# Performance work log

Measured on AMD Instinct MI355X. Metric: run time of the kernel, lower is better.

The kernel has to match this reference:

```python
import jax, jax.numpy as jnp
import numpy as np

B, L, H, NL = 4, 384, 128, 3
F = H * NL  # num_filters = hidden_dim * num_layers = h_V feature dim


def gelu(x):
    return jax.nn.gelu(x, approximate=False)  # torch nn.GELU default is exact erf


def setup_inputs() -> dict:
    key = jax.random.key(0)
    ks = jax.random.split(key, 10)
    rn = lambda k, shape, s=0.05: jax.random.normal(k, shape, jnp.float32) * s
    h_V = jax.random.normal(ks[0], (B, L, F), jnp.float32)
    h_E = jax.random.normal(ks[1], (B, L, L, H), jnp.float32)
    mask = (jax.random.uniform(ks[2], (B, L)) > 0.1).astype(jnp.float32)
    # CFConv filter_network: Linear(H->F), GELU, Linear(F->F), GELU
    fw1 = rn(ks[3], (H, F)); fb1 = jnp.zeros((F,), jnp.float32)
    fw2 = rn(ks[4], (F, F)); fb2 = jnp.zeros((F,), jnp.float32)
    # mlp_head: Linear(F->H), GELU, Linear(H->H//2), GELU, Linear(H//2->1)
    hw1 = rn(ks[5], (F, H)); hb1 = jnp.zeros((H,), jnp.float32)
    hw2 = rn(ks[6], (H, H // 2)); hb2 = jnp.zeros((H // 2,), jnp.float32)
    hw3 = rn(ks[7], (H // 2, 1)); hb3 = jnp.zeros((1,), jnp.float32)
    return dict(h_V=h_V, h_E=h_E, mask=mask, fw1=fw1, fb1=fb1, fw2=fw2, fb2=fb2,
                hw1=hw1, hb1=hb1, hw2=hw2, hb2=hb2, hw3=hw3, hb3=hb3)


def reference(h_V, h_E, mask, fw1, fb1, fw2, fb2, hw1, hb1, hw2, hb2, hw3, hb3):
    # CFConv: per-edge filter MLP on edge features [B,L,L,H] -> [B,L,L,F]
    Wf = gelu(gelu(h_E @ fw1 + fb1) @ fw2 + fb2)
    # broadcast multiply with x.unsqueeze(1) then sum over neighbor dim (dim=2)
    x_conv = jnp.einsum('bkf,blkf->blf', h_V, Wf)  # [B,L,F]
    # mlp_head (dropout is identity in eval)
    h = gelu(x_conv @ hw1 + hb1)
    h = gelu(h @ hw2 + hb2)
    pred = (h @ hw3 + hb3)[..., 0]  # [B,L]
    valid_length = jnp.clip(jnp.sum(mask, axis=1), 1.0, None)
    return jnp.sum(pred * mask, axis=1) / jnp.sqrt(valid_length)  # [B]
```

## Files before the change

### kernel.cpp

```cpp
#include <hip/hip_runtime.h>


#define Bz 4
#define Lz 384
#define Hz 128
#define Fz 384
#define KT 64
#define NIT 6
#define TILE_B (KT * Hz * 2)

typedef short bf16x8 __attribute__((ext_vector_type(8)));
typedef float f32x4 __attribute__((ext_vector_type(4)));

__device__ __forceinline__ unsigned short f2bf(float f) {
  unsigned int u = __float_as_uint(f);
  u += 0x7FFFu + ((u >> 16) & 1u);
  return (unsigned short)(u >> 16);
}

__device__ __forceinline__ float gelu_f(float x) {
  const float a1 = 0.254829592f, a2 = -0.284496736f, a3 = 1.421413741f;
  const float a4 = -1.453152027f, a5 = 1.061405429f;
  float z = fabsf(x) * 0.7071067811865476f;
  float t = __builtin_amdgcn_rcpf(__builtin_fmaf(0.3275911f, z, 1.0f));
  float poly = t * (a1 + t * (a2 + t * (a3 + t * (a4 + t * a5))));
  float e = __builtin_fmaf(-poly, __expf(-z * z), 1.0f);
  return 0.5f * x * (1.0f + copysignf(e, x));
}

__global__ __launch_bounds__(256) void prep_kernel(
    const float* __restrict__ fw1, const float* __restrict__ fw2,
    const float* __restrict__ hE,
    unsigned short* __restrict__ fw1P, unsigned short* __restrict__ fw2P,
    unsigned short* __restrict__ hEP,
    float* __restrict__ accbuf, int* __restrict__ ctr)
{
  int e = blockIdx.x * 256 + threadIdx.x;
  if (e < 16) accbuf[e] = 0.0f;
  if (e == 16) *ctr = 0;
  if (e < 24 * 4 * 64 * 8) {
    int j = e & 7, lf = (e >> 3) & 63, ks = (e >> 9) & 3, t = e >> 11;
    int n = t * 16 + (lf & 15);
    int k = ks * 32 + (lf >> 4) * 8 + j;
    fw1P[e] = f2bf(fw1[(size_t)k * Fz + n]);
  } else if (e < 24 * 4 * 64 * 8 + 24 * 12 * 64 * 8) {
    int o = e - 24 * 4 * 64 * 8;
    int j = o & 7, lf = (o >> 3) & 63, r = o >> 9;
    int ks = r % 12, t = r / 12;
    int n = t * 16 + (lf & 15);
    int k = ks * 32 + (lf >> 4) * 8 + j;
    fw2P[o] = f2bf(fw2[(size_t)k * Fz + n]);
  }
  if (e < Bz * Lz * NIT * KT * 16) {
    int u = e & 15;
    int r = (e >> 4) & 63;
    int tile = e >> 10;
    int it = tile % NIT;
    int bl = tile / NIT;
    const float* src = hE + (size_t)bl * (Lz * Hz)
                       + (size_t)(it * KT + r) * Hz + ((u ^ (r & 7)) << 3);
    f32x4 v0 = *(const f32x4*)src;
    f32x4 v1 = *(const f32x4*)(src + 4);
    bf16x8 o;
    o[0] = (short)f2bf(v0[0]); o[1] = (short)f2bf(v0[1]);
    o[2] = (short)f2bf(v0[2]); o[3] = (short)f2bf(v0[3]);
    o[4] = (short)f2bf(v1[0]); o[5] = (short)f2bf(v1[1]);
    o[6] = (short)f2bf(v1[2]); o[7] = (short)f2bf(v1[3]);
    *(bf16x8*)(hEP + (size_t)e * 8) = o;
  }
}

__global__ __launch_bounds__(512, 4) void schnet_main(
    const float* __restrict__ hV, const unsigned short* __restrict__ hEP,
    const float* __restrict__ mask,
    const unsigned short* __restrict__ fw1P, const float* __restrict__ fb1,
    const unsigned short* __restrict__ fw2P, const float* __restrict__ fb2,
    const float* __restrict__ hw1, const float* __restrict__ hb1,
    const float* __restrict__ hw2, const float* __restrict__ hb2,
    const float* __restrict__ hw3, const float* __restrict__ hb3,
    float* __restrict__ accbuf, int* __restrict__ ctr,
    float* __restrict__ out)
{
  const int bl   = blockIdx.x;
  const int b    = bl / Lz;
  const int l    = bl - b * Lz;
  const int tid  = threadIdx.x;
  const int wave = tid >> 6;
  const int lane = tid & 63;
  const int lr   = lane & 15;
  const int quad = lane >> 4;
  const int l7   = lane & 7;

  __shared__ __attribute__((aligned(16))) char sMem[65536];
  unsigned short* sA  = (unsigned short*)sMem;
  unsigned short* sT1 = (unsigned short*)(sMem + 16384);
  float* sXC = (float*)sMem;
  float* sHp = sXC + Fz;
  float* sH1 = sHp + 4 * Hz;
  float* sH2 = sH1 + Hz;
  int*   sLast = (int*)(sH2 + 64);

  const char* hEPt = (const char*)hEP + (size_t)bl * (NIT * TILE_B);
  const unsigned short* w1base = fw1P + (size_t)lane * 8;
  const unsigned short* w2base = fw2P + (size_t)lane * 8;

  const f32x4 zero4 = {0.f, 0.f, 0.f, 0.f};
  f32x4 xc[3];
  xc[0] = zero4; xc[1] = zero4; xc[2] = zero4;

  #pragma unroll
  for (int j = 0; j < 2; ++j) {
    int off = (j * 8 + wave) << 10;
    __builtin_amdgcn_global_load_lds(
        (const __attribute__((address_space(1))) void*)(hEPt + off + lane * 16),
        (__attribute__((address_space(3))) void*)(sMem + off), 16, 0, 0);
  }
  __syncthreads();

  for (int it = 0; it < NIT; ++it) {
    {
      f32x4 acc[4][3];
      #pragma unroll
      for (int mt = 0; mt < 4; ++mt)
        #pragma unroll
        for (int nt = 0; nt < 3; ++nt) acc[mt][nt] = zero4;

      #pragma unroll 2
      for (int ks = 0; ks < 4; ++ks) {
        const int xu = ((ks << 2) + quad) ^ l7;
        bf16x8 afr[4];
        #pragma unroll
        for (int mt = 0; mt < 4; ++mt)
          afr[mt] = *(const bf16x8*)(sA + ((mt * 16 + lr) << 7) + (xu << 3));
        bf16x8 bfr[3];
        #pragma unroll
        for (int nt = 0; nt < 3; ++nt)
          bfr[nt] = *(const bf16x8*)(w1base +
                        (size_t)(((wave * 3 + nt) * 4 + ks) * 64) * 8);
        __builtin_amdgcn_s_setprio(1);
        #pragma unroll
        for (int mt = 0; mt < 4; ++mt)
          #pragma unroll
          for (int nt = 0; nt < 3; ++nt)
            acc[mt][nt] = __builtin_amdgcn_mfma_f32_16x16x32_bf16(
                bfr[nt], afr[mt], acc[mt][nt], 0, 0, 0);
        __builtin_amdgcn_s_setprio(0);
      }
      #pragma unroll
      for (int nt = 0; nt < 3; ++nt) {
        const int n0 = wave * 48 + nt * 16 + quad * 4;
        const f32x4 bias = *(const f32x4*)(fb1 + n0);
        const int so = (((wave * 6 + nt * 2 + (quad >> 1)) ^ l7) << 3)
                       + ((quad & 1) << 2);
        #pragma unroll
        for (int mt = 0; mt < 4; ++mt) {
          short4 o;
          o.x = (short)f2bf(gelu_f(acc[mt][nt][0] + bias[0]));
          o.y = (short)f2bf(gelu_f(acc[mt][nt][1] + bias[1]));
          o.z = (short)f2bf(gelu_f(acc[mt][nt][2] + bias[2]));
          o.w = (short)f2bf(gelu_f(acc[mt][nt][3] + bias[3]));
          *(short4*)(sT1 + (mt * 16 + lr) * 384 + so) = o;
        }
      }
    }
    __syncthreads();

    if (it + 1 < NIT) {
      const char* gt = hEPt + (it + 1) * TILE_B;
      #pragma unroll
      for (int j = 0; j < 2; ++j) {
        int off = (j * 8 + wave) << 10;
        __builtin_amdgcn_global_load_lds(
            (const __attribute__((address_space(1))) void*)(gt + off + lane * 16),
            (__attribute__((address_space(3))) void*)(sMem + off), 16, 0, 0);
      }
    }

    {
      f32x4 acc[4][3];
      #pragma unroll
      for (int mt = 0; mt < 4; ++mt)
        #pragma unroll
        for (int nt = 0; nt < 3; ++nt) acc[mt][nt] = zero4;

      #pragma unroll 2
      for (int ks = 0; ks < 12; ++ks) {
        const int xu = ((ks << 2) + quad) ^ l7;
        bf16x8 afr[4];
        #pragma unroll
        for (int mt = 0; mt < 4; ++mt)
          afr[mt] = *(const bf16x8*)(sT1 + (mt * 16 + lr) * 384 + (xu << 3));
        bf16x8 bfr[3];
        #pragma unroll
        for (int nt = 0; nt < 3; ++nt)
          bfr[nt] = *(const bf16x8*)(w2base +
                        (size_t)(((wave * 3 + nt) * 12 + ks) * 64) * 8);
        __builtin_amdgcn_s_setprio(1);
        #pragma unroll
        for (int mt = 0; mt < 4; ++mt)
          #pragma unroll
          for (int nt = 0; nt < 3; ++nt)
            acc[mt][nt] = __builtin_amdgcn_mfma_f32_16x16x32_bf16(
                bfr[nt], afr[mt], acc[mt][nt], 0, 0, 0);
        __builtin_amdgcn_s_setprio(0);
      }
      #pragma unroll
      for (int nt = 0; nt < 3; ++nt) {
        const int n0 = wave * 48 + nt * 16 + quad * 4;
        const f32x4 b2 = *(const f32x4*)(fb2 + n0);
        #pragma unroll
        for (int mt = 0; mt < 4; ++mt) {
          const float* hv =
              hV + ((size_t)b * Lz + it * KT + mt * 16 + lr) * Fz + n0;
          const f32x4 hvv = *(const f32x4*)hv;
          #pragma unroll
          for (int r = 0; r < 4; ++r)
            xc[nt][r] += gelu_f(acc[mt][nt][r] + b2[r]) * hvv[r];
        }
      }
    }
    __syncthreads();
  }

  #pragma unroll
  for (int nt = 0; nt < 3; ++nt)
    #pragma unroll
    for (int r = 0; r < 4; ++r) {
      float v = xc[nt][r];
      v += __shfl_xor(v, 1);
      v += __shfl_xor(v, 2);
      v += __shfl_xor(v, 4);
      v += __shfl_xor(v, 8);
      if (lr == 0) sXC[wave * 48 + nt * 16 + quad * 4 + r] = v;
    }
  __syncthreads();

  {
    int i = tid & 127;
    int part = tid >> 7;
    float a = 0.f;
    const int f0 = part * 96;
    for (int f = f0; f < f0 + 96; ++f) a += sXC[f] * hw1[f * Hz + i];
    sHp[part * Hz + i] = a;
  }
  __syncthreads();
  if (tid < Hz)
    sH1[tid] = gelu_f(sHp[tid] + sHp[Hz + tid] + sHp[2 * Hz + tid]
                      + sHp[3 * Hz + tid] + hb1[tid]);
  __syncthreads();
  if (tid < 64) {
    float a = hb2[tid];
    for (int i = 0; i < Hz; ++i) a += sH1[i] * hw2[i * 64 + tid];
    sH2[tid] = gelu_f(a);
  }
  __syncthreads();
  if (wave == 0) {
    float v = sH2[lane] * hw3[lane];
    #pragma unroll
    for (int off = 32; off >= 1; off >>= 1) v += __shfl_xor(v, off);
    if (lane == 0) {
      float pred = v + hb3[0];
      atomicAdd(&accbuf[b], pred * mask[b * Lz + l]);
      __threadfence();
      *sLast = (atomicAdd(ctr, 1) == (Bz * Lz - 1));
    }
  }
  __syncthreads();

  if (*sLast && wave < Bz) {
    float s = 0.f;
    #pragma unroll
    for (int k = 0; k < Lz / 64; ++k) s += mask[wave * Lz + k * 64 + lane];
    #pragma unroll
    for (int off = 32; off >= 1; off >>= 1) s += __shfl_xor(s, off);
    if (lane == 0) {
      float vl = s < 1.0f ? 1.0f : s;
      float a = atomicAdd(&accbuf[wave], 0.0f);
      out[wave] = a / sqrtf(vl);
    }
  }
}

extern "C" void kernel_launch(void* const* d_in, const int* in_sizes, int n_in,
                              void* d_out, int out_size, void* d_ws, size_t ws_size,
                              hipStream_t stream)
{
  const float* hV   = (const float*)d_in[0];
  const float* hE   = (const float*)d_in[1];
  const float* mask = (const float*)d_in[2];
  const float* fw1  = (const float*)d_in[3];
  const float* fb1  = (const float*)d_in[4];
  const float* fw2  = (const float*)d_in[5];
  const float* fb2  = (const float*)d_in[6];
  const float* hw1  = (const float*)d_in[7];
  const float* hb1  = (const float*)d_in[8];
  const float* hw2  = (const float*)d_in[9];
  const float* hb2  = (const float*)d_in[10];
  const float* hw3  = (const float*)d_in[11];
  const float* hb3  = (const float*)d_in[12];
  float* out = (float*)d_out;

  float* accbuf = (float*)d_ws;
  int*   ctr    = (int*)((char*)d_ws + 64);
  unsigned short* fw1P = (unsigned short*)((char*)d_ws + 1024);
  unsigned short* fw2P = fw1P + 24 * 4 * 64 * 8;
  unsigned short* hEP  = fw2P + 24 * 12 * 64 * 8;

  const int units = Bz * Lz * NIT * KT * 16;
  prep_kernel<<<units / 256, 256, 0, stream>>>(fw1, fw2, hE, fw1P, fw2P, hEP,
                                               accbuf, ctr);
  schnet_main<<<Bz * Lz, 512, 0, stream>>>(hV, hEP, mask, fw1P, fb1, fw2P, fb2,
                                           hw1, hb1, hw2, hb2, hw3, hb3,
                                           accbuf, ctr, out);
}
```

Measured before the change: 875.6 us.

## Fuse h_E bf16 conversion into main kernel with register-staged prefetch

Removes the separate prep pass that converted the whole h_E tensor to a swizzled bf16 buffer. The main kernel now loads fp32 h_E directly, converts it to bf16 in registers and writes it to LDS. The load for the next tile is issued before the GEMM2 phase to hide its latency. The tile size is halved to 32 rows, with 12 iterations and half the LDS, which should allow more resident blocks but doubles the number of barriers and gives less MFMA work per wave per sync.

Result: faster. 844.3 us (-3.6%).

```diff
diff --git a/kernel.cpp b/kernel.cpp
--- a/kernel.cpp
+++ b/kernel.cpp
@@ -5,9 +5,8 @@
 #define Lz 384
 #define Hz 128
 #define Fz 384
-#define KT 64
-#define NIT 6
-#define TILE_B (KT * Hz * 2)
+#define KT 32
+#define NIT 12
 
 typedef short bf16x8 __attribute__((ext_vector_type(8)));
 typedef float f32x4 __attribute__((ext_vector_type(4)));
@@ -30,9 +29,7 @@
 
 __global__ __launch_bounds__(256) void prep_kernel(
     const float* __restrict__ fw1, const float* __restrict__ fw2,
-    const float* __restrict__ hE,
     unsigned short* __restrict__ fw1P, unsigned short* __restrict__ fw2P,
-    unsigned short* __restrict__ hEP,
     float* __restrict__ accbuf, int* __restrict__ ctr)
 {
   int e = blockIdx.x * 256 + threadIdx.x;
@@ -51,27 +48,10 @@
     int k = ks * 32 + (lf >> 4) * 8 + j;
     fw2P[o] = f2bf(fw2[(size_t)k * Fz + n]);
   }
-  if (e < Bz * Lz * NIT * KT * 16) {
-    int u = e & 15;
-    int r = (e >> 4) & 63;
-    int tile = e >> 10;
-    int it = tile % NIT;
-    int bl = tile / NIT;
-    const float* src = hE + (size_t)bl * (Lz * Hz)
-                       + (size_t)(it * KT + r) * Hz + ((u ^ (r & 7)) << 3);
-    f32x4 v0 = *(const f32x4*)src;
-    f32x4 v1 = *(const f32x4*)(src + 4);
-    bf16x8 o;
-    o[0] = (short)f2bf(v0[0]); o[1] = (short)f2bf(v0[1]);
-    o[2] = (short)f2bf(v0[2]); o[3] = (short)f2bf(v0[3]);
-    o[4] = (short)f2bf(v1[0]); o[5] = (short)f2bf(v1[1]);
-    o[6] = (short)f2bf(v1[2]); o[7] = (short)f2bf(v1[3]);
-    *(bf16x8*)(hEP + (size_t)e * 8) = o;
-  }
 }
 
 __global__ __launch_bounds__(512, 4) void schnet_main(
-    const float* __restrict__ hV, const unsigned short* __restrict__ hEP,
+    const float* __restrict__ hV, const float* __restrict__ hE,
     const float* __restrict__ mask,
     const unsigned short* __restrict__ fw1P, const float* __restrict__ fb1,
     const unsigned short* __restrict__ fw2P, const float* __restrict__ fb2,
@@ -91,133 +71,146 @@
   const int quad = lane >> 4;
   const int l7   = lane & 7;
 
-  __shared__ __attribute__((aligned(16))) char sMem[65536];
+  __shared__ __attribute__((aligned(16))) char sMem[32768];
   unsigned short* sA  = (unsigned short*)sMem;
-  unsigned short* sT1 = (unsigned short*)(sMem + 16384);
+  unsigned short* sT1 = (unsigned short*)(sMem + 8192);
   float* sXC = (float*)sMem;
   float* sHp = sXC + Fz;
   float* sH1 = sHp + 4 * Hz;
   float* sH2 = sH1 + Hz;
   int*   sLast = (int*)(sH2 + 64);
 
-  const char* hEPt = (const char*)hEP + (size_t)bl * (NIT * TILE_B);
+  const float* hE_bl = hE + (size_t)bl * (Lz * Hz);
   const unsigned short* w1base = fw1P + (size_t)lane * 8;
   const unsigned short* w2base = fw2P + (size_t)lane * 8;
+
+  const int srow = tid >> 4;
+  const int su   = tid & 15;
+  const float* hE_stage = hE_bl + (size_t)tid * 8;
+  unsigned short* sAw = sA + srow * 128 + (((su ^ (srow & 7)) & 15) << 3);
 
   const f32x4 zero4 = {0.f, 0.f, 0.f, 0.f};
   f32x4 xc[3];
   xc[0] = zero4; xc[1] = zero4; xc[2] = zero4;
 
-  #pragma unroll
-  for (int j = 0; j < 2; ++j) {
-    int off = (j * 8 + wave) << 10;
-    __builtin_amdgcn_global_load_lds(
-        (const __attribute__((address_space(1))) void*)(hEPt + off + lane * 16),
-        (__attribute__((address_space(3))) void*)(sMem + off), 16, 0, 0);
-  }
-  __syncthreads();
-
+  {
+    f32x4 v0 = *(const f32x4*)hE_stage;
+    f32x4 v1 = *(const f32x4*)(hE_stage + 4);
+    bf16x8 o;
+    o[0] = (short)f2bf(v0[0]); o[1] = (short)f2bf(v0[1]);
+    o[2] = (short)f2bf(v0[2]); o[3] = (short)f2bf(v0[3]);
+    o[4] = (short)f2bf(v1[0]); o[5] = (short)f2bf(v1[1]);
+    o[6] = (short)f2bf(v1[2]); o[7] = (short)f2bf(v1[3]);
+    *(bf16x8*)sAw = o;
+  }
+  __syncthreads();
+
+  #pragma unroll 1
   for (int it = 0; it < NIT; ++it) {
-    {
-      f32x4 acc[4][3];
-      #pragma unroll
-      for (int mt = 0; mt < 4; ++mt)
-        #pragma unroll
-        for (int nt = 0; nt < 3; ++nt) acc[mt][nt] = zero4;
-
-      #pragma unroll 2
-      for (int ks = 0; ks < 4; ++ks) {
-        const int xu = ((ks << 2) + quad) ^ l7;
-        bf16x8 afr[4];
-        #pragma unroll
-        for (int mt = 0; mt < 4; ++mt)
-          afr[mt] = *(const bf16x8*)(sA + ((mt * 16 + lr) << 7) + (xu << 3));
-        bf16x8 bfr[3];
+    f32x4 s0, s1;
+
+    f32x4 acc1[2][3];
+    #pragma unroll
+    for (int mt = 0; mt < 2; ++mt)
+      #pragma unroll
+      for (int nt = 0; nt < 3; ++nt) acc1[mt][nt] = zero4;
+
+    #pragma unroll 2
+    for (int ks = 0; ks < 4; ++ks) {
+      const int xu = ((ks << 2) + quad) ^ l7;
+      bf16x8 afr[2];
+      #pragma unroll
+      for (int mt = 0; mt < 2; ++mt)
+        afr[mt] = *(const bf16x8*)(sA + ((mt * 16 + lr) << 7) + (xu << 3));
+      bf16x8 bfr[3];
+      #pragma unroll
+      for (int nt = 0; nt < 3; ++nt)
+        bfr[nt] = *(const bf16x8*)(w1base +
+                      (size_t)(((wave * 3 + nt) * 4 + ks) * 64) * 8);
+      __builtin_amdgcn_s_setprio(1);
+      #pragma unroll
+      for (int mt = 0; mt < 2; ++mt)
         #pragma unroll
         for (int nt = 0; nt < 3; ++nt)
-          bfr[nt] = *(const bf16x8*)(w1base +
-                        (size_t)(((wave * 3 + nt) * 4 + ks) * 64) * 8);
-        __builtin_amdgcn_s_setprio(1);
-        #pragma unroll
-        for (int mt = 0; mt < 4; ++mt)
-          #pragma unroll
-          for (int nt = 0; nt < 3; ++nt)
-            acc[mt][nt] = __builtin_amdgcn_mfma_f32_16x16x32_bf16(
-                bfr[nt], afr[mt], acc[mt][nt], 0, 0, 0);
-        __builtin_amdgcn_s_setprio(0);
+          acc1[mt][nt] = __builtin_amdgcn_mfma_f32_16x16x32_bf16(
+              bfr[nt], afr[mt], acc1[mt][nt], 0, 0, 0);
+      __builtin_amdgcn_s_setprio(0);
+    }
+
+    if (it + 1 < NIT) {
+      const float* src = hE_stage + (size_t)(it + 1) * (KT * Hz);
+      s0 = *(const f32x4*)src;
+      s1 = *(const f32x4*)(src + 4);
+    }
+
+    #pragma unroll
+    for (int nt = 0; nt < 3; ++nt) {
+      const int n0 = wave * 48 + nt * 16 + quad * 4;
+      const f32x4 bias = *(const f32x4*)(fb1 + n0);
+      const int so = (((wave * 6 + nt * 2 + (quad >> 1)) ^ l7) << 3)
+                     + ((quad & 1) << 2);
+      #pragma unroll
+      for (int mt = 0; mt < 2; ++mt) {
+        short4 o;
+        o.x = (short)f2bf(gelu_f(acc1[mt][nt][0] + bias[0]));
+        o.y = (short)f2bf(gelu_f(acc1[mt][nt][1] + bias[1]));
+        o.z = (short)f2bf(gelu_f(acc1[mt][nt][2] + bias[2]));
+        o.w = (short)f2bf(gelu_f(acc1[mt][nt][3] + bias[3]));
+        *(short4*)(sT1 + (mt * 16 + lr) * 384 + so) = o;
       }
-      #pragma unroll
-      for (int nt = 0; nt < 3; ++nt) {
-        const int n0 = wave * 48 + nt * 16 + quad * 4;
-        const f32x4 bias = *(const f32x4*)(fb1 + n0);
-        const int so = (((wave * 6 + nt * 2 + (quad >> 1)) ^ l7) << 3)
-                       + ((quad & 1) << 2);
-        #pragma unroll
-        for (int mt = 0; mt < 4; ++mt) {
-          short4 o;
-          o.x = (short)f2bf(gelu_f(acc[mt][nt][0] + bias[0]));
-          o.y = (short)f2bf(gelu_f(acc[mt][nt][1] + bias[1]));
-          o.z = (short)f2bf(gelu_f(acc[mt][nt][2] + bias[2]));
-          o.w = (short)f2bf(gelu_f(acc[mt][nt][3] + bias[3]));
-          *(short4*)(sT1 + (mt * 16 + lr) * 384 + so) = o;
-        }
-      }
     }
     __syncthreads();
 
-    if (it + 1 < NIT) {
-      const char* gt = hEPt + (it + 1) * TILE_B;
-      #pragma unroll
-      for (int j = 0; j < 2; ++j) {
-        int off = (j * 8 + wave) << 10;
-        __builtin_amdgcn_global_load_lds(
-            (const __attribute__((address_space(1))) void*)(gt + off + lane * 16),
-            (__attribute__((address_space(3))) void*)(sMem + off), 16, 0, 0);
-      }
-    }
-
-    {
-      f32x4 acc[4][3];
-      #pragma unroll
-      for (int mt = 0; mt < 4; ++mt)
-        #pragma unroll
-        for (int nt = 0; nt < 3; ++nt) acc[mt][nt] = zero4;
-
-      #pragma unroll 2
-      for (int ks = 0; ks < 12; ++ks) {
-        const int xu = ((ks << 2) + quad) ^ l7;
-        bf16x8 afr[4];
-        #pragma unroll
-        for (int mt = 0; mt < 4; ++mt)
-          afr[mt] = *(const bf16x8*)(sT1 + (mt * 16 + lr) * 384 + (xu << 3));
-        bf16x8 bfr[3];
+    f32x4 acc2[2][3];
+    #pragma unroll
+    for (int mt = 0; mt < 2; ++mt)
+      #pragma unroll
+      for (int nt = 0; nt < 3; ++nt) acc2[mt][nt] = zero4;
+
+    #pragma unroll 2
+    for (int ks = 0; ks < 12; ++ks) {
+      const int xu = ((ks << 2) + quad) ^ l7;
+      bf16x8 afr[2];
+      #pragma unroll
+      for (int mt = 0; mt < 2; ++mt)
+        afr[mt] = *(const bf16x8*)(sT1 + (mt * 16 + lr) * 384 + (xu << 3));
+      bf16x8 bfr[3];
+      #pragma unroll
+      for (int nt = 0; nt < 3; ++nt)
+        bfr[nt] = *(const bf16x8*)(w2base +
+                      (size_t)(((wave * 3 + nt) * 12 + ks) * 64) * 8);
+      __builtin_amdgcn_s_setprio(1);
+      #pragma unroll
+      for (int mt = 0; mt < 2; ++mt)
         #pragma unroll
         for (int nt = 0; nt < 3; ++nt)
-          bfr[nt] = *(const bf16x8*)(w2base +
-                        (size_t)(((wave * 3 + nt) * 12 + ks) * 64) * 8);
-        __builtin_amdgcn_s_setprio(1);
+          acc2[mt][nt] = __builtin_amdgcn_mfma_f32_16x16x32_bf16(
+              bfr[nt], afr[mt], acc2[mt][nt], 0, 0, 0);
+      __builtin_amdgcn_s_setprio(0);
+    }
+
+    #pragma unroll
+    for (int nt = 0; nt < 3; ++nt) {
+      const int n0 = wave * 48 + nt * 16 + quad * 4;
+      const f32x4 b2 = *(const f32x4*)(fb2 + n0);
+      #pragma unroll
+      for (int mt = 0; mt < 2; ++mt) {
+        const float* hv =
+            hV + ((size_t)b * Lz + it * KT + mt * 16 + lr) * Fz + n0;
+        const f32x4 hvv = *(const f32x4*)hv;
         #pragma unroll
-        for (int mt = 0; mt < 4; ++mt)
-          #pragma unroll
-          for (int nt = 0; nt < 3; ++nt)
-            acc[mt][nt] = __builtin_amdgcn_mfma_f32_16x16x32_bf16(
-                bfr[nt], afr[mt], acc[mt][nt], 0, 0, 0);
-        __builtin_amdgcn_s_setprio(0);
+        for (int r = 0; r < 4; ++r)
+          xc[nt][r] += gelu_f(acc2[mt][nt][r] + b2[r]) * hvv[r];
       }
-      #pragma unroll
-      for (int nt = 0; nt < 3; ++nt) {
-        const int n0 = wave * 48 + nt * 16 + quad * 4;
-        const f32x4 b2 = *(const f32x4*)(fb2 + n0);
-        #pragma unroll
-        for (int mt = 0; mt < 4; ++mt) {
-          const float* hv =
-              hV + ((size_t)b * Lz + it * KT + mt * 16 + lr) * Fz + n0;
-          const f32x4 hvv = *(const f32x4*)hv;
-          #pragma unroll
-          for (int r = 0; r < 4; ++r)
-            xc[nt][r] += gelu_f(acc[mt][nt][r] + b2[r]) * hvv[r];
-        }
-      }
+    }
+
+    if (it + 1 < NIT) {
+      bf16x8 o;
+      o[0] = (short)f2bf(s0[0]); o[1] = (short)f2bf(s0[1]);
+      o[2] = (short)f2bf(s0[2]); o[3] = (short)f2bf(s0[3]);
+      o[4] = (short)f2bf(s1[0]); o[5] = (short)f2bf(s1[1]);
+      o[6] = (short)f2bf(s1[2]); o[7] = (short)f2bf(s1[3]);
+      *(bf16x8*)sAw = o;
     }
     __syncthreads();
   }
@@ -304,12 +297,9 @@
   int*   ctr    = (int*)((char*)d_ws + 64);
   unsigned short* fw1P = (unsigned short*)((char*)d_ws + 1024);
   unsigned short* fw2P = fw1P + 24 * 4 * 64 * 8;
-  unsigned short* hEP  = fw2P + 24 * 12 * 64 * 8;
-
-  const int units = Bz * Lz * NIT * KT * 16;
-  prep_kernel<<<units / 256, 256, 0, stream>>>(fw1, fw2, hE, fw1P, fw2P, hEP,
-                                               accbuf, ctr);
-  schnet_main<<<Bz * Lz, 512, 0, stream>>>(hV, hEP, mask, fw1P, fb1, fw2P, fb2,
+
+  prep_kernel<<<768, 256, 0, stream>>>(fw1, fw2, fw1P, fw2P, accbuf, ctr);
+  schnet_main<<<Bz * Lz, 512, 0, stream>>>(hV, hE, mask, fw1P, fb1, fw2P, fb2,
                                            hw1, hb1, hw2, hb2, hw3, hb3,
                                            accbuf, ctr, out);
 }
```
